# Performance work log

Hardware: AMD Instinct MI355X
Metric: run time of the kernel (lower is better)

## Reference

```python
import jax, jax.numpy as jnp
import numpy as np

INIT_STDEV = 0.01

def setup_inputs() -> dict:
    key = jax.random.key(0)
    k1, k2, k3 = jax.random.split(key, 3)
    B, S, D = 8, 4096, 768
    x = jax.random.normal(k1, (B, S, D), dtype=jnp.float32)
    att_v = jax.random.normal(k2, (D,), dtype=jnp.float32) * INIT_STDEV
    att_W = jax.random.normal(k3, (D, D), dtype=jnp.float32) * INIT_STDEV
    return {"x": x, "att_v": att_v, "att_W": att_W}

def reference(x, att_v, att_W):
    # y = x @ W : [B,S,D]; scores = tanh(y) . v over D : [B,S]
    y = jnp.tanh(jnp.einsum('bsd,de->bse', x, att_W))
    scores = jnp.einsum('bsd,d->bs', y, att_v)
    weights = jax.nn.softmax(scores, axis=-1)            # softmax over sequence
    out = jnp.einsum('bs,bsd->bd', weights, x)           # attsum pool
    return out.astype(jnp.float32)
```

## Files before the change

kernel.cpp:

```cpp
#include <hip/hip_runtime.h>
#include <hip/hip_bf16.h>

constexpr int Bb = 8;
constexpr int Ss = 4096;
constexpr int Dd = 768;
constexpr int Mm = Bb * Ss;

typedef __bf16 bf16x8 __attribute__((ext_vector_type(8)));
typedef float f32x4 __attribute__((ext_vector_type(4)));

__device__ __forceinline__ float fast_tanh(float x) {
    return 1.f - 2.f / (__expf(2.f * x) + 1.f);
}

__device__ __forceinline__ void load_lds16(const void* g, void* l) {
    __builtin_amdgcn_global_load_lds(
        (const __attribute__((address_space(1))) unsigned int*)g,
        (__attribute__((address_space(3))) unsigned int*)l, 16, 0, 0);
}

__global__ __launch_bounds__(256) void convWX(const float* __restrict__ W,
                                              __bf16* __restrict__ Wt,
                                              const float* __restrict__ x,
                                              __bf16* __restrict__ xb) {
    const int bid = blockIdx.x;
    if (bid < 576) {
        __shared__ float tile[32][33];
        const int tx = threadIdx.x & 31;
        const int ty = threadIdx.x >> 5;
        const int kb = (bid % 24) * 32;
        const int nb = (bid / 24) * 32;
#pragma unroll
        for (int i = 0; i < 32; i += 8)
            tile[ty + i][tx] = W[(size_t)(kb + ty + i) * Dd + nb + tx];
        __syncthreads();
#pragma unroll
        for (int i = 0; i < 32; i += 8) {
            const int n = nb + ty + i;
            const int txs = (tx & 7) | ((((tx >> 3) & 3) ^ ((n >> 1) & 3)) << 3);
            Wt[(size_t)n * Dd + kb + txs] = (__bf16)tile[tx][ty + i];
        }
    } else {
        const size_t i = ((size_t)(bid - 576) * 256 + threadIdx.x) * 8;
        const float4 a = *(const float4*)(x + i);
        const float4 b = *(const float4*)(x + i + 4);
        bf16x8 p;
        p[0] = (__bf16)a.x; p[1] = (__bf16)a.y; p[2] = (__bf16)a.z; p[3] = (__bf16)a.w;
        p[4] = (__bf16)b.x; p[5] = (__bf16)b.y; p[6] = (__bf16)b.z; p[7] = (__bf16)b.w;
        *(bf16x8*)(xb + i) = p;
    }
}

__global__ __launch_bounds__(512, 4) void scores_gemm(
    const __bf16* __restrict__ xb, const __bf16* __restrict__ Wt,
    const float* __restrict__ v, float* __restrict__ scores3) {
    __shared__ __bf16 As[3][128 * 32];
    __shared__ __bf16 Bs[3][256 * 32];
    __shared__ float ssc[8][64];

    const int t = threadIdx.x;
    const int id = blockIdx.x;
    const int ids = ((id & 7) * 96) + (id >> 3);
    const int mb = ids / 3;
    const int nb = ids - mb * 3;
    const int lane = t & 63;
    const int wave = t >> 6;
    const int wm = wave >> 2;
    const int wn = wave & 3;
    const int quad = lane >> 4;
    const int lid = lane & 15;
    const int rslot = ((quad ^ ((lid >> 1) & 3)) * 8);

    const __bf16* axg = xb + (size_t)(mb * 128 + (t >> 2)) * Dd + (t & 3) * 8;
    const int awl = t * 8;

    const __bf16* bgp[2];
    int blp[2];
#pragma unroll
    for (int j = 0; j < 2; ++j) {
        const int flat = j * 8192 + t * 16;
        const int col = flat >> 6;
        bgp[j] = Wt + (size_t)(nb * 256 + col) * Dd + ((flat & 63) >> 1);
        blp[j] = flat >> 1;
    }

    f32x4 acc[4][4];
#pragma unroll
    for (int tm = 0; tm < 4; ++tm)
#pragma unroll
        for (int nt = 0; nt < 4; ++nt) acc[tm][nt] = (f32x4){0.f, 0.f, 0.f, 0.f};

    load_lds16(axg, &As[0][awl]);
#pragma unroll
    for (int j = 0; j < 2; ++j) load_lds16(bgp[j], &Bs[0][blp[j]]);
    load_lds16(axg + 32, &As[1][awl]);
#pragma unroll
    for (int j = 0; j < 2; ++j) load_lds16(bgp[j] + 32, &Bs[1][blp[j]]);

#pragma unroll
    for (int k = 0; k < 24; ++k) {
        if (k == 23) asm volatile("s_waitcnt vmcnt(0)" ::: "memory");
        else         asm volatile("s_waitcnt vmcnt(3)" ::: "memory");
        __builtin_amdgcn_sched_barrier(0);
        __builtin_amdgcn_s_barrier();
        __builtin_amdgcn_sched_barrier(0);

        if (k < 22) {
            load_lds16(axg + (k + 2) * 32, &As[(k + 2) % 3][awl]);
#pragma unroll
            for (int j = 0; j < 2; ++j)
                load_lds16(bgp[j] + (k + 2) * 32, &Bs[(k + 2) % 3][blp[j]]);
        }
        __builtin_amdgcn_sched_barrier(0);

        bf16x8 af[4], bfr[4];
#pragma unroll
        for (int tm = 0; tm < 4; ++tm)
            af[tm] = *(const bf16x8*)(&As[k % 3][(wm * 64 + tm * 16 + lid) * 32 + quad * 8]);
#pragma unroll
        for (int nt = 0; nt < 4; ++nt)
            bfr[nt] = *(const bf16x8*)(&Bs[k % 3][(wn * 64 + nt * 16 + lid) * 32 + rslot]);

        __builtin_amdgcn_s_setprio(1);
#pragma unroll
        for (int tm = 0; tm < 4; ++tm)
#pragma unroll
            for (int nt = 0; nt < 4; ++nt)
                acc[tm][nt] = __builtin_amdgcn_mfma_f32_16x16x32_bf16(af[tm], bfr[nt], acc[tm][nt], 0, 0, 0);
        __builtin_amdgcn_s_setprio(0);
    }

    float vv[4];
#pragma unroll
    for (int nt = 0; nt < 4; ++nt)
        vv[nt] = v[nb * 256 + wn * 64 + nt * 16 + lid];

#pragma unroll
    for (int tm = 0; tm < 4; ++tm)
#pragma unroll
        for (int r = 0; r < 4; ++r) {
            float s = 0.f;
#pragma unroll
            for (int nt = 0; nt < 4; ++nt) s += vv[nt] * fast_tanh(acc[tm][nt][r]);
            s += __shfl_xor(s, 1);
            s += __shfl_xor(s, 2);
            s += __shfl_xor(s, 4);
            s += __shfl_xor(s, 8);
            if (lid == 0) ssc[wave][tm * 16 + quad * 4 + r] = s;
        }
    __syncthreads();
    if (t < 128) {
        const int wmh = t >> 6;
        const int rl = t & 63;
        float s = 0.f;
#pragma unroll
        for (int ww = 0; ww < 4; ++ww) s += ssc[wmh * 4 + ww][rl];
        scores3[(size_t)nb * Mm + mb * 128 + t] = s;
    }
}

__global__ __launch_bounds__(192) void pool1e(const float* __restrict__ x,
                                              const float* __restrict__ scores3,
                                              float* __restrict__ partial,
                                              float* __restrict__ esum) {
    const int b = blockIdx.y;
    const int c = blockIdx.x;
    const int t = threadIdx.x;
    __shared__ float we[32];

    if (t < 32) {
        const size_t i = (size_t)b * Ss + c * 32 + t;
        we[t] = __expf(scores3[i] + scores3[Mm + i] + scores3[2 * Mm + i]);
    }
    __syncthreads();

    const float* base = x + ((size_t)b * Ss + c * 32) * Dd;
    float4 acc = make_float4(0.f, 0.f, 0.f, 0.f);
#pragma unroll 8
    for (int i = 0; i < 32; ++i) {
        const float ww = we[i];
        const float4 xv = *(const float4*)(base + (size_t)i * Dd + t * 4);
        acc.x += ww * xv.x;
        acc.y += ww * xv.y;
        acc.z += ww * xv.z;
        acc.w += ww * xv.w;
    }
    *(float4*)(partial + ((size_t)(b * 128 + c)) * Dd + t * 4) = acc;
    if (t == 0) {
        float s = 0.f;
#pragma unroll
        for (int i = 0; i < 32; ++i) s += we[i];
        esum[b * 128 + c] = s;
    }
}

__global__ __launch_bounds__(128) void pool2(const float* __restrict__ partial,
                                             const float* __restrict__ esum,
                                             float* __restrict__ out) {
    const int b = blockIdx.y;
    const int t = threadIdx.x;
    const int d = blockIdx.x * 128 + t;

    float es = 0.f;
    if (t < 64) {
        es = esum[b * 128 + t] + esum[b * 128 + 64 + t];
        es += __shfl_xor(es, 1);
        es += __shfl_xor(es, 2);
        es += __shfl_xor(es, 4);
        es += __shfl_xor(es, 8);
        es += __shfl_xor(es, 16);
        es += __shfl_xor(es, 32);
    }
    __shared__ float esT;
    if (t == 0) esT = es;
    __syncthreads();
    const float inv = 1.f / esT;

    float s = 0.f;
#pragma unroll 8
    for (int c = 0; c < 128; ++c) s += partial[((size_t)(b * 128 + c)) * Dd + d];
    out[(size_t)b * Dd + d] = s * inv;
}

extern "C" void kernel_launch(void* const* d_in, const int* in_sizes, int n_in,
                              void* d_out, int out_size, void* d_ws, size_t ws_size,
                              hipStream_t stream) {
    (void)in_sizes; (void)n_in; (void)ws_size; (void)out_size;
    const float* x = (const float*)d_in[0];
    const float* v = (const float*)d_in[1];
    const float* W = (const float*)d_in[2];

    char* ws = (char*)d_ws;
    constexpr size_t OFF_WT = 0;
    constexpr size_t OFF_SC = 1179648;
    constexpr size_t OFF_ES = OFF_SC + 393216;
    constexpr size_t OFF_PA = OFF_ES + 4096;
    constexpr size_t OFF_XB = OFF_PA + 3145728;

    __bf16* Wt     = (__bf16*)(ws + OFF_WT);
    float* scores3 = (float*)(ws + OFF_SC);
    float* esum    = (float*)(ws + OFF_ES);
    float* partial = (float*)(ws + OFF_PA);
    __bf16* xb     = (__bf16*)(ws + OFF_XB);

    convWX<<<dim3(576 + (Mm * Dd) / (256 * 8)), 256, 0, stream>>>(W, Wt, x, xb);
    scores_gemm<<<dim3(3 * Mm / 128), 512, 0, stream>>>(xb, Wt, v, scores3);
    pool1e<<<dim3(128, Bb), 192, 0, stream>>>(x, scores3, partial, esum);
    pool2<<<dim3(6, Bb), 128, 0, stream>>>(partial, esum, (float*)d_out);
}
```

Measured before the change: 226.5 us.

## Swizzle bf16 x layout for conflict-free LDS reads and pool from bf16 copy

Result: faster. 219.9 us (-2.9%).

```diff
diff --git a/kernel.cpp b/kernel.cpp
--- a/kernel.cpp
+++ b/kernel.cpp
@@ -7,6 +7,7 @@
 constexpr int Mm = Bb * Ss;
 
 typedef __bf16 bf16x8 __attribute__((ext_vector_type(8)));
+typedef __bf16 bf16x4 __attribute__((ext_vector_type(4)));
 typedef float f32x4 __attribute__((ext_vector_type(4)));
 
 __device__ __forceinline__ float fast_tanh(float x) {
@@ -42,12 +43,16 @@
         }
     } else {
         const size_t i = ((size_t)(bid - 576) * 256 + threadIdx.x) * 8;
+        const int m = (int)(i / Dd);
+        const int k = (int)(i % Dd);
+        const int sl = (k >> 3) & 3;
+        const int dk = (k & ~31) | (((sl ^ ((m >> 1) & 3)) << 3));
         const float4 a = *(const float4*)(x + i);
         const float4 b = *(const float4*)(x + i + 4);
         bf16x8 p;
         p[0] = (__bf16)a.x; p[1] = (__bf16)a.y; p[2] = (__bf16)a.z; p[3] = (__bf16)a.w;
         p[4] = (__bf16)b.x; p[5] = (__bf16)b.y; p[6] = (__bf16)b.z; p[7] = (__bf16)b.w;
-        *(bf16x8*)(xb + i) = p;
+        *(bf16x8*)(xb + (size_t)m * Dd + dk) = p;
     }
 }
 
@@ -116,7 +121,7 @@
         bf16x8 af[4], bfr[4];
 #pragma unroll
         for (int tm = 0; tm < 4; ++tm)
-            af[tm] = *(const bf16x8*)(&As[k % 3][(wm * 64 + tm * 16 + lid) * 32 + quad * 8]);
+            af[tm] = *(const bf16x8*)(&As[k % 3][(wm * 64 + tm * 16 + lid) * 32 + rslot]);
 #pragma unroll
         for (int nt = 0; nt < 4; ++nt)
             bfr[nt] = *(const bf16x8*)(&Bs[k % 3][(wn * 64 + nt * 16 + lid) * 32 + rslot]);
@@ -159,7 +164,7 @@
     }
 }
 
-__global__ __launch_bounds__(192) void pool1e(const float* __restrict__ x,
+__global__ __launch_bounds__(192) void pool1e(const __bf16* __restrict__ xb,
                                               const float* __restrict__ scores3,
                                               float* __restrict__ partial,
                                               float* __restrict__ esum) {
@@ -174,18 +179,25 @@
     }
     __syncthreads();
 
-    const float* base = x + ((size_t)b * Ss + c * 32) * Dd;
+    const int d0 = t * 4;
+    const int kc = d0 & ~31;
+    const int sl = (d0 >> 3) & 3;
+    const int w8 = d0 & 7;
+    const int m0 = b * Ss + c * 32;
+    const __bf16* base = xb + (size_t)m0 * Dd;
+
     float4 acc = make_float4(0.f, 0.f, 0.f, 0.f);
 #pragma unroll 8
     for (int i = 0; i < 32; ++i) {
         const float ww = we[i];
-        const float4 xv = *(const float4*)(base + (size_t)i * Dd + t * 4);
-        acc.x += ww * xv.x;
-        acc.y += ww * xv.y;
-        acc.z += ww * xv.z;
-        acc.w += ww * xv.w;
-    }
-    *(float4*)(partial + ((size_t)(b * 128 + c)) * Dd + t * 4) = acc;
+        const int phys = kc + ((sl ^ (((m0 + i) >> 1) & 3)) << 3) + w8;
+        const bf16x4 xv = *(const bf16x4*)(base + (size_t)i * Dd + phys);
+        acc.x += ww * (float)xv[0];
+        acc.y += ww * (float)xv[1];
+        acc.z += ww * (float)xv[2];
+        acc.w += ww * (float)xv[3];
+    }
+    *(float4*)(partial + ((size_t)(b * 128 + c)) * Dd + d0) = acc;
     if (t == 0) {
         float s = 0.f;
 #pragma unroll
@@ -245,6 +257,6 @@
 
     convWX<<<dim3(576 + (Mm * Dd) / (256 * 8)), 256, 0, stream>>>(W, Wt, x, xb);
     scores_gemm<<<dim3(3 * Mm / 128), 512, 0, stream>>>(xb, Wt, v, scores3);
-    pool1e<<<dim3(128, Bb), 192, 0, stream>>>(x, scores3, partial, esum);
+    pool1e<<<dim3(128, Bb), 192, 0, stream>>>(xb, scores3, partial, esum);
     pool2<<<dim3(6, Bb), 128, 0, stream>>>(partial, esum, (float*)d_out);
 }
```
